# Optimization experiments

Hardware: AMD Instinct MI355X
Metric: run time of the kernel (lower is better)

The kernel has to match this reference:

```python
import jax, jax.numpy as jnp
import numpy as np

L = 8      # subsequence_len
A = 4      # alphabet_size
D = 256    # sketch_dim
SEQ = 16384


def setup_inputs() -> dict:
    key = jax.random.key(0)
    k1, k2, k3 = jax.random.split(key, 3)
    sequence = jax.random.randint(k1, (SEQ,), 0, A)
    # stacked nn.Embedding weights: (L, A, D), init N(0, 0.5)
    hash_emb = 0.5 * jax.random.normal(k2, (L, A, D), dtype=jnp.float32)
    sign_logits = 0.5 * jax.random.normal(k3, (L, A), dtype=jnp.float32)
    return {"sequence": sequence, "hash_emb": hash_emb, "sign_logits": sign_logits}


def _forward(sequence, hash_emb, sign_logits):
    # roll_idx[j, s] = (j - s) % D  so that gather reproduces torch.roll(t, s)[j] = t[(j - s) % D]
    roll_idx = (jnp.arange(D)[:, None] - jnp.arange(D)[None, :]) % D
    p_arr = jnp.arange(1, L + 1, dtype=jnp.float32)           # p = 1..L
    Tp0 = jnp.zeros((L + 1, D), dtype=jnp.float32).at[0, 0].set(1.0)
    Tm0 = jnp.zeros((L + 1, D), dtype=jnp.float32)

    def step(carry, xs):
        Tp, Tm = carry                                         # (L+1, D) each
        c, i = xs
        valid = (c >= 0) & (c < A)
        c_safe = jnp.clip(c, 0, A - 1)
        # eval-mode soft hash: softmax over the embedding row (per level p)
        probs = jax.nn.softmax(hash_emb[:, c_safe, :], axis=-1)   # (L, D)
        sign = jax.nn.sigmoid(sign_logits[:, c_safe])             # (L,)
        denom = (i + 1).astype(jnp.float32)
        # z = p/(i+1); levels with p > i+1 (and invalid chars) are frozen (z=0)
        z = jnp.where((p_arr <= denom) & valid, p_arr / denom, 0.0)  # (L,)
        Tp_prev, Tm_prev = Tp[:L], Tm[:L]                         # (L, D)
        # expected circular shift: out[l, j] = sum_s probs[l, s] * T_prev[l, (j-s)%D]
        stp = jnp.einsum('ljs,ls->lj', Tp_prev[:, roll_idx], probs)
        stm = jnp.einsum('ljs,ls->lj', Tm_prev[:, roll_idx], probs)
        s = sign[:, None]
        upd_p = s * stp + (1.0 - s) * stm
        upd_m = s * stm + (1.0 - s) * stp
        zc = z[:, None]
        new_Tp = Tp.at[1:].set((1.0 - zc) * Tp[1:] + zc * upd_p)
        new_Tm = Tm.at[1:].set((1.0 - zc) * Tm[1:] + zc * upd_m)
        return (new_Tp, new_Tm), None

    step = jax.checkpoint(step)
    (Tp, Tm), _ = jax.lax.scan(step, (Tp0, Tm0), (sequence, jnp.arange(SEQ)))
    return Tp[L] - Tm[L]


def reference(sequence, hash_emb, sign_logits):
    return _forward(sequence, hash_emb, sign_logits)
```

## Files before the change

kernel.cpp:

```cpp
#include <hip/hip_runtime.h>
#include <math.h>

#define LL 8
#define AA 4
#define DD 256
#define KF 129
#define KH 128
#define CLEN 16
#define NES 36
#define LPAD 37

typedef float v2f __attribute__((ext_vector_type(2)));

#define SIX(l2,l1) ((((l2)*((l2)-1))>>1) + (l1))
#define SLOT(s)    ((s)*LPAD + ((s)>>1))

#define V_OFF   0
#define VP_OFF  (2*KF)
#define CNT_OFF (VP_OFF + 128*4*NES*2)

__device__ __forceinline__ float invCN8() {
  constexpr double c = (16384.0 * 16383.0 * 16382.0 * 16381.0 *
                        16380.0 * 16379.0 * 16378.0 * 16377.0) / 40320.0;
  return (float)(1.0 / c);
}

template <bool R2>
__device__ __forceinline__ v2f opfma(const v2f b, const v2f a, v2f acc) {
  if (R2) {
    return __builtin_elementwise_fma(b, a, acc);
  } else {
    const v2f bb = (v2f){ b.x,  b.x};
    const v2f bw = (v2f){-b.y,  b.y};
    const v2f as = (v2f){ a.y,  a.x};
    acc = __builtin_elementwise_fma(bb, a,  acc);
    acc = __builtin_elementwise_fma(bw, as, acc);
    return acc;
  }
}

template <unsigned MASK, bool R2>
__device__ __forceinline__ void prodCols(const v2f* __restrict__ A, const v2f* __restrict__ B,
                                         v2f (&o)[NES]) {
#pragma unroll
  for (int l1 = 0; l1 < 8; ++l1) {
    if ((MASK >> l1) & 1) {
#pragma unroll
      for (int l2 = l1 + 1; l2 <= 8; ++l2) {
        v2f acc = A[SIX(l2, l1)] + B[SIX(l2, l1)];
#pragma unroll
        for (int m = l1 + 1; m < l2; ++m) acc = opfma<R2>(B[SIX(l2, m)], A[SIX(m, l1)], acc);
        o[SIX(l2, l1)] = acc;
      }
    }
  }
}

template <unsigned MASK>
__device__ __forceinline__ void writeCols(v2f* __restrict__ D, const v2f (&o)[NES]) {
#pragma unroll
  for (int l1 = 0; l1 < 8; ++l1) {
    if ((MASK >> l1) & 1) {
#pragma unroll
      for (int l2 = l1 + 1; l2 <= 8; ++l2) D[SIX(l2, l1)] = o[SIX(l2, l1)];
    }
  }
}

template <bool R2>
__device__ __forceinline__ void prodFullRA(const v2f (&A)[NES], const v2f* __restrict__ B,
                                           v2f (&o)[NES]) {
#pragma unroll
  for (int l1 = 0; l1 < 8; ++l1) {
#pragma unroll
    for (int l2 = l1 + 1; l2 <= 8; ++l2) {
      v2f acc = A[SIX(l2, l1)] + B[SIX(l2, l1)];
#pragma unroll
      for (int m = l1 + 1; m < l2; ++m) acc = opfma<R2>(B[SIX(l2, m)], A[SIX(m, l1)], acc);
      o[SIX(l2, l1)] = acc;
    }
  }
}

template <bool R2>
__device__ __forceinline__ void applyOp(v2f (&s)[LL + 1], const v2f* __restrict__ op) {
#pragma unroll
  for (int l2 = LL; l2 >= 1; --l2) {
    v2f acc = s[l2];
#pragma unroll
    for (int m = 0; m < l2; ++m) acc = opfma<R2>(op[SIX(l2, m)], s[m], acc);
    s[l2] = acc;
  }
}

template <bool R2>
__device__ __forceinline__ void bodyMain(const int* __restrict__ seq, v2f* L,
                                         const float4* qtab, int t, int qtr) {
  v2f G[NES];
#pragma unroll
  for (int e = 0; e < NES; ++e) G[e] = (v2f){0.f, 0.f};

  const int ch = qtr * 256 + t;
  const int4* sp = (const int4*)(seq + ch * CLEN);
  for (int sb = 0; sb < CLEN / 4; ++sb) {
    const int4 cs = sp[sb];
    const int csy[4] = {cs.x, cs.y, cs.z, cs.w};
#pragma unroll
    for (int u = 0; u < 4; ++u) {
      const int c = csy[u];
      float4 qv[LL];
#pragma unroll
      for (int l = 0; l < LL; ++l) qv[l] = qtab[(l << 2) | c];
#pragma unroll
      for (int l = LL; l >= 1; --l) {
        const float4 q4 = qv[l - 1];
        if (R2) {
          const v2f qa = (v2f){q4.x, q4.y};
          G[SIX(l, l - 1)] += qa;
#pragma unroll
          for (int l1 = 0; l1 < l - 1; ++l1)
            G[SIX(l, l1)] = __builtin_elementwise_fma(qa, G[SIX(l - 1, l1)], G[SIX(l, l1)]);
        } else {
          const v2f qa = (v2f){q4.x, q4.y};
          const v2f qb = (v2f){q4.z, q4.w};
          { v2f g = G[SIX(l, l - 1)]; g.x += q4.x; g.y += q4.w; G[SIX(l, l - 1)] = g; }
#pragma unroll
          for (int l1 = 0; l1 < l - 1; ++l1) {
            const v2f H  = G[SIX(l - 1, l1)];
            const v2f Hs = (v2f){H.y, H.x};
            v2f g = G[SIX(l, l1)];
            g = __builtin_elementwise_fma(qa, H,  g);
            g = __builtin_elementwise_fma(qb, Hs, g);
            G[SIX(l, l1)] = g;
          }
        }
      }
    }
  }

  if (t & 1) {
    v2f* D = L + SLOT(t >> 1);
#pragma unroll
    for (int e = 0; e < NES; ++e) D[e] = G[e];
  }
  __syncthreads();
  if (!(t & 1)) {
    v2f o[NES];
    prodFullRA<R2>(G, L + SLOT(t >> 1), o);
    v2f* D = L + SLOT(t >> 1);
#pragma unroll
    for (int e = 0; e < NES; ++e) D[e] = o[e];
  }
  __syncthreads();

  const int w = t >> 6;
  const int j = t & 63;
  v2f pc[NES];
  for (int n = 64; n >= 1; n >>= 1) {
    const bool act = (j < n);
    if (act) {
      const v2f* Ab = L + SLOT(2 * j);
      const v2f* Bb = L + SLOT(2 * j + 1);
      switch (w) {
        case 0:  prodCols<0x01, R2>(Ab, Bb, pc); break;
        case 1:  prodCols<0x42, R2>(Ab, Bb, pc); break;
        case 2:  prodCols<0x14, R2>(Ab, Bb, pc); break;
        default: prodCols<0xA8, R2>(Ab, Bb, pc); break;
      }
    }
    __syncthreads();
    if (act) {
      v2f* Db = L + SLOT(j);
      switch (w) {
        case 0:  writeCols<0x01>(Db, pc); break;
        case 1:  writeCols<0x42>(Db, pc); break;
        case 2:  writeCols<0x14>(Db, pc); break;
        default: writeCols<0xA8>(Db, pc); break;
      }
    }
    __syncthreads();
  }
}

__global__ __launch_bounds__(256) void kmain(const int* __restrict__ seq,
                                             const float* __restrict__ hemb,
                                             const float* __restrict__ slog,
                                             float* __restrict__ v,
                                             float* __restrict__ vpart,
                                             int* __restrict__ cnt,
                                             float* __restrict__ outp) {
  const int blk = blockIdx.x;
  const int k   = blk >> 2;
  const int qtr = blk & 3;
  const int t   = threadIdx.x;
  __shared__ __align__(16) float ldsf[9600];
  __shared__ __align__(16) float4 qtab[LL * AA];
  __shared__ float2 twd[256];
  __shared__ float dvr[KF], dvi[KF];
  __shared__ int isLast, isPairLast;

  {
    float sn, cs;
    __sincosf((float)t * 0.0245436926061702596754894014319f, &sn, &cs);
    twd[t] = make_float2(cs, sn);
  }
  __syncthreads();

  {
    const int r  = t >> 3;
    const int g8 = t & 7;
    float4 hv[8];
#pragma unroll
    for (int u = 0; u < 8; ++u)
      hv[u] = *(const float4*)(hemb + r * DD + u * 32 + g8 * 4);
    float mx = -1e30f;
#pragma unroll
    for (int u = 0; u < 8; ++u)
      mx = fmaxf(mx, fmaxf(fmaxf(hv[u].x, hv[u].y), fmaxf(hv[u].z, hv[u].w)));
    mx = fmaxf(mx, __shfl_xor(mx, 1));
    mx = fmaxf(mx, __shfl_xor(mx, 2));
    mx = fmaxf(mx, __shfl_xor(mx, 4));

    float sum = 0.f, cr = 0.f, ci = 0.f;
    if (k > 0) {
#pragma unroll
      for (int u = 0; u < 8; ++u) {
        const float ev[4] = {expf(hv[u].x - mx), expf(hv[u].y - mx),
                             expf(hv[u].z - mx), expf(hv[u].w - mx)};
#pragma unroll
        for (int w2 = 0; w2 < 4; ++w2) {
          const int jj = u * 32 + g8 * 4 + w2;
          const int m = (jj * k) & 255;
          const float2 tv = twd[m];
          sum += ev[w2];
          cr = fmaf(ev[w2], tv.x, cr);
          ci = fmaf(-ev[w2], tv.y, ci);
        }
      }
    } else {
#pragma unroll
      for (int u = 0; u < 8; ++u) {
        const float ev[4] = {expf(hv[u].x - mx), expf(hv[u].y - mx),
                             expf(hv[u].z - mx), expf(hv[u].w - mx)};
        sum += ev[0] + ev[1] + ev[2] + ev[3];
        cr  += (ev[0] - ev[1]) + (ev[2] - ev[3]);
      }
    }
    sum += __shfl_xor(sum, 1); cr += __shfl_xor(cr, 1); ci += __shfl_xor(ci, 1);
    sum += __shfl_xor(sum, 2); cr += __shfl_xor(cr, 2); ci += __shfl_xor(ci, 2);
    sum += __shfl_xor(sum, 4); cr += __shfl_xor(cr, 4); ci += __shfl_xor(ci, 4);

    if (g8 == 0) {
      const float sl = slog[r];
      const float sg = 1.0f / (1.0f + expf(-sl));
      const float q  = fmaf(2.0f, sg, -1.0f);
      if (k > 0) {
        const float qr = cr * q / sum;
        const float qi = ci * q / sum;
        qtab[r] = make_float4(qr, qr, -qi, qi);
      } else {
        qtab[r] = make_float4(q, cr * q / sum, 0.f, 0.f);
      }
    }
  }
  __syncthreads();

  v2f* L = (v2f*)ldsf;
  if (k == 0) bodyMain<true>(seq, L, qtab, t, qtr);
  else        bodyMain<false>(seq, L, qtab, t, qtr);

  if (t < NES) {
    union { v2f v2; double d; } u;
    u.v2 = L[t];
    __hip_atomic_store((double*)vpart + (size_t)(k * 4 + qtr) * NES + t, u.d,
                       __ATOMIC_RELEASE, __HIP_MEMORY_SCOPE_AGENT);
  }
  __syncthreads();
  if (t == 0) {
    const int old = __hip_atomic_fetch_add(&cnt[1 + k], 1, __ATOMIC_ACQ_REL, __HIP_MEMORY_SCOPE_AGENT);
    isPairLast = (old == 3) ? 1 : 0;
  }
  __syncthreads();
  if (isPairLast) {
    if (t < 4 * NES) {
      union { v2f v2; double d; } u;
      u.d = __hip_atomic_load((const double*)vpart + (size_t)(k * 4) * NES + t,
                              __ATOMIC_ACQUIRE, __HIP_MEMORY_SCOPE_AGENT);
      L[t] = u.v2;
    }
    __syncthreads();
    if (t == 0) {
      v2f s[LL + 1];
      s[0] = (k == 0) ? (v2f){1.f, 1.f} : (v2f){1.f, 0.f};
#pragma unroll
      for (int l = 1; l <= LL; ++l) s[l] = (v2f){0.f, 0.f};
      for (int qq = 0; qq < 4; ++qq) {
        const v2f* op = L + qq * NES;
        if (k == 0) applyOp<true>(s, op); else applyOp<false>(s, op);
      }
      if (k == 0) {
        __hip_atomic_store(&v[0],          s[LL].x, __ATOMIC_RELEASE, __HIP_MEMORY_SCOPE_AGENT);
        __hip_atomic_store(&v[1],          0.0f,    __ATOMIC_RELEASE, __HIP_MEMORY_SCOPE_AGENT);
        __hip_atomic_store(&v[2 * KH],     s[LL].y, __ATOMIC_RELEASE, __HIP_MEMORY_SCOPE_AGENT);
        __hip_atomic_store(&v[2 * KH + 1], 0.0f,    __ATOMIC_RELEASE, __HIP_MEMORY_SCOPE_AGENT);
      } else {
        __hip_atomic_store(&v[2 * k],     s[LL].x, __ATOMIC_RELEASE, __HIP_MEMORY_SCOPE_AGENT);
        __hip_atomic_store(&v[2 * k + 1], s[LL].y, __ATOMIC_RELEASE, __HIP_MEMORY_SCOPE_AGENT);
      }
      __hip_atomic_store(&cnt[1 + k], 0, __ATOMIC_RELAXED, __HIP_MEMORY_SCOPE_AGENT);
    }
  }

  __syncthreads();
  if (t == 0) {
    const int old = __hip_atomic_fetch_add(&cnt[0], 1, __ATOMIC_ACQ_REL, __HIP_MEMORY_SCOPE_AGENT);
    isLast = (old == 511) ? 1 : 0;
  }
  __syncthreads();
  if (isLast) {
    if (t < KF) {
      dvr[t] = __hip_atomic_load(&v[2 * t],     __ATOMIC_ACQUIRE, __HIP_MEMORY_SCOPE_AGENT);
      dvi[t] = __hip_atomic_load(&v[2 * t + 1], __ATOMIC_ACQUIRE, __HIP_MEMORY_SCOPE_AGENT);
    }
    if (t == 0)
      __hip_atomic_store(&cnt[0], 0, __ATOMIC_RELEASE, __HIP_MEMORY_SCOPE_AGENT);
    __syncthreads();
    const float sc = (1.0f / 256.0f) * invCN8();
    float sum = dvr[0] + ((t & 1) ? -dvr[KH] : dvr[KH]);
    for (int k2 = 1; k2 < KH; ++k2) {
      const int m = (t * k2) & 255;
      const float2 wv = twd[m];
      sum = fmaf(2.0f * dvr[k2], wv.x, sum);
      sum = fmaf(-2.0f * dvi[k2], wv.y, sum);
    }
    outp[t] = sum * sc;
  }
}

extern "C" void kernel_launch(void* const* d_in, const int* in_sizes, int n_in,
                              void* d_out, int out_size, void* d_ws, size_t ws_size,
                              hipStream_t stream) {
  (void)in_sizes; (void)n_in; (void)out_size; (void)ws_size;
  const int*   seq  = (const int*)d_in[0];
  const float* hemb = (const float*)d_in[1];
  const float* slog = (const float*)d_in[2];
  float* ws    = (float*)d_ws;
  float* v     = ws + V_OFF;
  float* vpart = ws + VP_OFF;
  int*   cnt   = (int*)(ws + CNT_OFF);
  float* o     = (float*)d_out;

  hipMemsetAsync(cnt, 0, (1 + KH) * sizeof(int), stream);
  hipLaunchKernelGGL(kmain, dim3(512), dim3(256), 0, stream, seq, hemb, slog, v, vpart, cnt, o);
}
```

Measured before the change: 114.3 us.

## Split each frequency across two 512-thread blocks instead of four 256-thread blocks

Each frequency k now uses two blocks of 512 threads rather than four blocks of 256, so the sequence is split into halves. The in-block tree reduction of transfer operators gains one more level and LDS usage doubles. The cross-block combine now handles two partial operators and is done by a wavefront using shuffles instead of a single thread. This cuts cross-block atomic traffic and serial combine work, at the cost of more LDS per block, fewer blocks, and a deeper reduction with more syncthreads.

```diff
diff --git a/kernel.cpp b/kernel.cpp
--- a/kernel.cpp
+++ b/kernel.cpp
@@ -6,6 +6,7 @@
 #define DD 256
 #define KF 129
 #define KH 128
+#define THR 512
 #define CLEN 16
 #define NES 36
 #define LPAD 37
@@ -16,8 +17,8 @@
 #define SLOT(s)    ((s)*LPAD + ((s)>>1))
 
 #define V_OFF   0
-#define VP_OFF  (2*KF)
-#define CNT_OFF (VP_OFF + 128*4*NES*2)
+#define VP_OFF  (2 * KF)
+#define CNT_OFF (VP_OFF + 128 * 2 * NES * 2)
 
 __device__ __forceinline__ float invCN8() {
   constexpr double c = (16384.0 * 16383.0 * 16382.0 * 16381.0 *
@@ -83,25 +84,13 @@
 }
 
 template <bool R2>
-__device__ __forceinline__ void applyOp(v2f (&s)[LL + 1], const v2f* __restrict__ op) {
-#pragma unroll
-  for (int l2 = LL; l2 >= 1; --l2) {
-    v2f acc = s[l2];
-#pragma unroll
-    for (int m = 0; m < l2; ++m) acc = opfma<R2>(op[SIX(l2, m)], s[m], acc);
-    s[l2] = acc;
-  }
-}
-
-template <bool R2>
 __device__ __forceinline__ void bodyMain(const int* __restrict__ seq, v2f* L,
-                                         const float4* qtab, int t, int qtr) {
+                                         const float4* qtab, int t, int half) {
   v2f G[NES];
 #pragma unroll
   for (int e = 0; e < NES; ++e) G[e] = (v2f){0.f, 0.f};
 
-  const int ch = qtr * 256 + t;
-  const int4* sp = (const int4*)(seq + ch * CLEN);
+  const int4* sp = (const int4*)(seq + half * (THR * CLEN) + t * CLEN);
   for (int sb = 0; sb < CLEN / 4; ++sb) {
     const int4 cs = sp[sb];
     const int csy[4] = {cs.x, cs.y, cs.z, cs.w};
@@ -153,10 +142,10 @@
   }
   __syncthreads();
 
-  const int w = t >> 6;
-  const int j = t & 63;
+  const int w = t >> 7;
+  const int j = t & 127;
   v2f pc[NES];
-  for (int n = 64; n >= 1; n >>= 1) {
+  for (int n = 128; n >= 1; n >>= 1) {
     const bool act = (j < n);
     if (act) {
       const v2f* Ab = L + SLOT(2 * j);
@@ -182,24 +171,24 @@
   }
 }
 
-__global__ __launch_bounds__(256) void kmain(const int* __restrict__ seq,
-                                             const float* __restrict__ hemb,
-                                             const float* __restrict__ slog,
-                                             float* __restrict__ v,
-                                             float* __restrict__ vpart,
-                                             int* __restrict__ cnt,
-                                             float* __restrict__ outp) {
-  const int blk = blockIdx.x;
-  const int k   = blk >> 2;
-  const int qtr = blk & 3;
-  const int t   = threadIdx.x;
-  __shared__ __align__(16) float ldsf[9600];
+__global__ __launch_bounds__(THR, 1) void kmain(const int* __restrict__ seq,
+                                                const float* __restrict__ hemb,
+                                                const float* __restrict__ slog,
+                                                float* __restrict__ v,
+                                                float* __restrict__ vpart,
+                                                int* __restrict__ cnt,
+                                                float* __restrict__ outp) {
+  const int blk  = blockIdx.x;
+  const int k    = blk >> 1;
+  const int half = blk & 1;
+  const int t    = threadIdx.x;
+  __shared__ __align__(16) float ldsf[19200];
   __shared__ __align__(16) float4 qtab[LL * AA];
   __shared__ float2 twd[256];
   __shared__ float dvr[KF], dvi[KF];
-  __shared__ int isLast, isPairLast;
-
-  {
+  __shared__ int isLast, isPair;
+
+  if (t < 256) {
     float sn, cs;
     __sincosf((float)t * 0.0245436926061702596754894014319f, &sn, &cs);
     twd[t] = make_float2(cs, sn);
@@ -207,29 +196,30 @@
   __syncthreads();
 
   {
-    const int r  = t >> 3;
-    const int g8 = t & 7;
-    float4 hv[8];
-#pragma unroll
-    for (int u = 0; u < 8; ++u)
-      hv[u] = *(const float4*)(hemb + r * DD + u * 32 + g8 * 4);
+    const int r   = t >> 4;
+    const int g16 = t & 15;
+    float4 hv[4];
+#pragma unroll
+    for (int u = 0; u < 4; ++u)
+      hv[u] = *(const float4*)(hemb + r * DD + u * 64 + g16 * 4);
     float mx = -1e30f;
 #pragma unroll
-    for (int u = 0; u < 8; ++u)
+    for (int u = 0; u < 4; ++u)
       mx = fmaxf(mx, fmaxf(fmaxf(hv[u].x, hv[u].y), fmaxf(hv[u].z, hv[u].w)));
     mx = fmaxf(mx, __shfl_xor(mx, 1));
     mx = fmaxf(mx, __shfl_xor(mx, 2));
     mx = fmaxf(mx, __shfl_xor(mx, 4));
+    mx = fmaxf(mx, __shfl_xor(mx, 8));
 
     float sum = 0.f, cr = 0.f, ci = 0.f;
     if (k > 0) {
 #pragma unroll
-      for (int u = 0; u < 8; ++u) {
+      for (int u = 0; u < 4; ++u) {
         const float ev[4] = {expf(hv[u].x - mx), expf(hv[u].y - mx),
                              expf(hv[u].z - mx), expf(hv[u].w - mx)};
 #pragma unroll
         for (int w2 = 0; w2 < 4; ++w2) {
-          const int jj = u * 32 + g8 * 4 + w2;
+          const int jj = u * 64 + g16 * 4 + w2;
           const int m = (jj * k) & 255;
           const float2 tv = twd[m];
           sum += ev[w2];
@@ -239,7 +229,7 @@
       }
     } else {
 #pragma unroll
-      for (int u = 0; u < 8; ++u) {
+      for (int u = 0; u < 4; ++u) {
         const float ev[4] = {expf(hv[u].x - mx), expf(hv[u].y - mx),
                              expf(hv[u].z - mx), expf(hv[u].w - mx)};
         sum += ev[0] + ev[1] + ev[2] + ev[3];
@@ -249,8 +239,9 @@
     sum += __shfl_xor(sum, 1); cr += __shfl_xor(cr, 1); ci += __shfl_xor(ci, 1);
     sum += __shfl_xor(sum, 2); cr += __shfl_xor(cr, 2); ci += __shfl_xor(ci, 2);
     sum += __shfl_xor(sum, 4); cr += __shfl_xor(cr, 4); ci += __shfl_xor(ci, 4);
-
-    if (g8 == 0) {
+    sum += __shfl_xor(sum, 8); cr += __shfl_xor(cr, 8); ci += __shfl_xor(ci, 8);
+
+    if (g16 == 0) {
       const float sl = slog[r];
       const float sg = 1.0f / (1.0f + expf(-sl));
       const float q  = fmaf(2.0f, sg, -1.0f);
@@ -266,55 +257,73 @@
   __syncthreads();
 
   v2f* L = (v2f*)ldsf;
-  if (k == 0) bodyMain<true>(seq, L, qtab, t, qtr);
-  else        bodyMain<false>(seq, L, qtab, t, qtr);
+  if (k == 0) bodyMain<true>(seq, L, qtab, t, half);
+  else        bodyMain<false>(seq, L, qtab, t, half);
 
   if (t < NES) {
     union { v2f v2; double d; } u;
     u.v2 = L[t];
-    __hip_atomic_store((double*)vpart + (size_t)(k * 4 + qtr) * NES + t, u.d,
+    __hip_atomic_store((double*)vpart + (size_t)(k * 2 + half) * NES + t, u.d,
                        __ATOMIC_RELEASE, __HIP_MEMORY_SCOPE_AGENT);
   }
   __syncthreads();
   if (t == 0) {
     const int old = __hip_atomic_fetch_add(&cnt[1 + k], 1, __ATOMIC_ACQ_REL, __HIP_MEMORY_SCOPE_AGENT);
-    isPairLast = (old == 3) ? 1 : 0;
-  }
-  __syncthreads();
-  if (isPairLast) {
-    if (t < 4 * NES) {
+    isPair = (old == 1) ? 1 : 0;
+  }
+  __syncthreads();
+  if (isPair) {
+    if (t < 2 * NES) {
       union { v2f v2; double d; } u;
-      u.d = __hip_atomic_load((const double*)vpart + (size_t)(k * 4) * NES + t,
+      u.d = __hip_atomic_load((const double*)vpart + (size_t)(k * 2) * NES + t,
                               __ATOMIC_ACQUIRE, __HIP_MEMORY_SCOPE_AGENT);
       L[t] = u.v2;
     }
     __syncthreads();
-    if (t == 0) {
-      v2f s[LL + 1];
-      s[0] = (k == 0) ? (v2f){1.f, 1.f} : (v2f){1.f, 0.f};
-#pragma unroll
-      for (int l = 1; l <= LL; ++l) s[l] = (v2f){0.f, 0.f};
-      for (int qq = 0; qq < 4; ++qq) {
-        const v2f* op = L + qq * NES;
-        if (k == 0) applyOp<true>(s, op); else applyOp<false>(s, op);
-      }
-      if (k == 0) {
-        __hip_atomic_store(&v[0],          s[LL].x, __ATOMIC_RELEASE, __HIP_MEMORY_SCOPE_AGENT);
-        __hip_atomic_store(&v[1],          0.0f,    __ATOMIC_RELEASE, __HIP_MEMORY_SCOPE_AGENT);
-        __hip_atomic_store(&v[2 * KH],     s[LL].y, __ATOMIC_RELEASE, __HIP_MEMORY_SCOPE_AGENT);
-        __hip_atomic_store(&v[2 * KH + 1], 0.0f,    __ATOMIC_RELEASE, __HIP_MEMORY_SCOPE_AGENT);
-      } else {
-        __hip_atomic_store(&v[2 * k],     s[LL].x, __ATOMIC_RELEASE, __HIP_MEMORY_SCOPE_AGENT);
-        __hip_atomic_store(&v[2 * k + 1], s[LL].y, __ATOMIC_RELEASE, __HIP_MEMORY_SCOPE_AGENT);
-      }
-      __hip_atomic_store(&cnt[1 + k], 0, __ATOMIC_RELAXED, __HIP_MEMORY_SCOPE_AGENT);
+    if (t < 64) {
+      v2f sv[LL + 1];
+      sv[0] = (k == 0) ? (v2f){1.f, 1.f} : (v2f){1.f, 0.f};
+#pragma unroll
+      for (int l = 1; l <= LL; ++l) sv[l] = (v2f){0.f, 0.f};
+      for (int gg = 0; gg < 2; ++gg) {
+        v2f nv = (v2f){0.f, 0.f};
+        if (t >= 1 && t <= LL) {
+          nv = sv[t];
+          const v2f* Bb = L + gg * NES;
+          const int rb = (t * (t - 1)) >> 1;
+#pragma unroll
+          for (int l1 = 0; l1 < 8; ++l1) {
+            if (l1 < t) {
+              if (k == 0) nv = __builtin_elementwise_fma(Bb[rb + l1], sv[l1], nv);
+              else        nv = opfma<false>(Bb[rb + l1], sv[l1], nv);
+            }
+          }
+        }
+#pragma unroll
+        for (int l = 1; l <= LL; ++l) {
+          sv[l].x = __shfl(nv.x, l);
+          sv[l].y = __shfl(nv.y, l);
+        }
+      }
+      if (t == 0) {
+        if (k == 0) {
+          __hip_atomic_store(&v[0],          sv[LL].x, __ATOMIC_RELEASE, __HIP_MEMORY_SCOPE_AGENT);
+          __hip_atomic_store(&v[1],          0.0f,     __ATOMIC_RELEASE, __HIP_MEMORY_SCOPE_AGENT);
+          __hip_atomic_store(&v[2 * KH],     sv[LL].y, __ATOMIC_RELEASE, __HIP_MEMORY_SCOPE_AGENT);
+          __hip_atomic_store(&v[2 * KH + 1], 0.0f,     __ATOMIC_RELEASE, __HIP_MEMORY_SCOPE_AGENT);
+        } else {
+          __hip_atomic_store(&v[2 * k],     sv[LL].x, __ATOMIC_RELEASE, __HIP_MEMORY_SCOPE_AGENT);
+          __hip_atomic_store(&v[2 * k + 1], sv[LL].y, __ATOMIC_RELEASE, __HIP_MEMORY_SCOPE_AGENT);
+        }
+        __hip_atomic_store(&cnt[1 + k], 0, __ATOMIC_RELAXED, __HIP_MEMORY_SCOPE_AGENT);
+      }
     }
   }
 
   __syncthreads();
   if (t == 0) {
     const int old = __hip_atomic_fetch_add(&cnt[0], 1, __ATOMIC_ACQ_REL, __HIP_MEMORY_SCOPE_AGENT);
-    isLast = (old == 511) ? 1 : 0;
+    isLast = (old == 255) ? 1 : 0;
   }
   __syncthreads();
   if (isLast) {
@@ -325,15 +334,17 @@
     if (t == 0)
       __hip_atomic_store(&cnt[0], 0, __ATOMIC_RELEASE, __HIP_MEMORY_SCOPE_AGENT);
     __syncthreads();
-    const float sc = (1.0f / 256.0f) * invCN8();
-    float sum = dvr[0] + ((t & 1) ? -dvr[KH] : dvr[KH]);
-    for (int k2 = 1; k2 < KH; ++k2) {
-      const int m = (t * k2) & 255;
-      const float2 wv = twd[m];
-      sum = fmaf(2.0f * dvr[k2], wv.x, sum);
-      sum = fmaf(-2.0f * dvi[k2], wv.y, sum);
-    }
-    outp[t] = sum * sc;
+    if (t < 256) {
+      const float sc = (1.0f / 256.0f) * invCN8();
+      float sum = dvr[0] + ((t & 1) ? -dvr[KH] : dvr[KH]);
+      for (int k2 = 1; k2 < KH; ++k2) {
+        const int m = (t * k2) & 255;
+        const float2 wv = twd[m];
+        sum = fmaf(2.0f * dvr[k2], wv.x, sum);
+        sum = fmaf(-2.0f * dvi[k2], wv.y, sum);
+      }
+      outp[t] = sum * sc;
+    }
   }
 }
 
@@ -351,5 +362,5 @@
   float* o     = (float*)d_out;
 
   hipMemsetAsync(cnt, 0, (1 + KH) * sizeof(int), stream);
-  hipLaunchKernelGGL(kmain, dim3(512), dim3(256), 0, stream, seq, hemb, slog, v, vpart, cnt, o);
-}
+  hipLaunchKernelGGL(kmain, dim3(256), dim3(THR), 0, stream, seq, hemb, slog, v, vpart, cnt, o);
+}
```

Result: faster. 101.1 us (-11.6%).
